# Kernel tuning notes

Measured on AMD Instinct MI355X. Metric: run time of the kernel, lower is better.

## Reference

```python
import math
import jax, jax.numpy as jnp
import numpy as np

SCORE_THR = 0.05
NMS_THR = 0.5
MIN_SIZE = 0.01
MAX_DET = 100
SCALE_CLAMP = math.log(1000.0 / 16.0)
WX, WY, WW, WH = 10.0, 10.0, 5.0, 5.0  # BoxCoder weights


def setup_inputs() -> dict:
    key = jax.random.key(0)
    k1, k2, k3, k4 = jax.random.split(key, 4)
    B, N, C = 4, 2048, 3
    H = W = 800
    class_logits = 2.0 * jax.random.normal(k1, (B, N, C), dtype=jnp.float32)
    box_regression = 0.5 * jax.random.normal(k2, (B, N, 4 * C), dtype=jnp.float32)
    cxy = jax.random.uniform(k3, (B, N, 2), minval=0.0, maxval=float(W))
    wh = jax.random.uniform(k4, (B, N, 2), minval=4.0, maxval=100.0)
    proposals = jnp.concatenate([cxy - 0.5 * wh, cxy + 0.5 * wh], axis=-1)
    proposals = jnp.clip(proposals, 0.0, float(W))
    return {"class_logits": class_logits, "box_regression": box_regression,
            "proposals": proposals, "image_h": H, "image_w": W}


def _decode(rel, props):
    # rel: [N, C, 4] deltas, props: [N, 4] xyxy -> [N, C, 4] decoded boxes
    w = props[:, 2] - props[:, 0]
    h = props[:, 3] - props[:, 1]
    cx = props[:, 0] + 0.5 * w
    cy = props[:, 1] + 0.5 * h
    dx = rel[..., 0] / WX
    dy = rel[..., 1] / WY
    dw = jnp.minimum(rel[..., 2] / WW, SCALE_CLAMP)
    dh = jnp.minimum(rel[..., 3] / WH, SCALE_CLAMP)
    pcx = dx * w[:, None] + cx[:, None]
    pcy = dy * h[:, None] + cy[:, None]
    pw = jnp.exp(dw) * w[:, None]
    ph = jnp.exp(dh) * h[:, None]
    return jnp.stack([pcx - 0.5 * pw, pcy - 0.5 * ph,
                      pcx + 0.5 * pw, pcy + 0.5 * ph], axis=-1)


def _pairwise_iou(b):
    # b: [M, 4] -> [M, M]
    area = (b[:, 2] - b[:, 0]) * (b[:, 3] - b[:, 1])
    lt = jnp.maximum(b[:, None, :2], b[None, :, :2])
    rb = jnp.minimum(b[:, None, 2:], b[None, :, 2:])
    whd = jnp.clip(rb - lt, 0.0)
    inter = whd[..., 0] * whd[..., 1]
    return inter / (area[:, None] + area[None, :] - inter + 1e-7)


def _per_image(logits, rel, props, H, W):
    N, C = logits.shape
    scores = jax.nn.softmax(logits, axis=-1)               # [N, C]
    boxes = _decode(rel.reshape(N, C, 4), props)           # [N, C, 4]
    # clip to image (x in [0,W], y in [0,H])
    boxes = jnp.stack([jnp.clip(boxes[..., 0], 0.0, W),
                       jnp.clip(boxes[..., 1], 0.0, H),
                       jnp.clip(boxes[..., 2], 0.0, W),
                       jnp.clip(boxes[..., 3], 0.0, H)], axis=-1)
    # drop background class and flatten -> M = N*(C-1)
    boxes = boxes[:, 1:, :].reshape(-1, 4)
    scores = scores[:, 1:].reshape(-1)
    labels = jnp.broadcast_to(jnp.arange(1, C), (N, C - 1)).reshape(-1)
    valid = ((scores > SCORE_THR)
             & (boxes[:, 2] - boxes[:, 0] >= MIN_SIZE)
             & (boxes[:, 3] - boxes[:, 1] >= MIN_SIZE))
    # batched_nms via per-class coordinate offset
    offset = labels.astype(boxes.dtype) * (jnp.max(boxes) + 1.0)
    ob = boxes + offset[:, None]
    sort_key = jnp.where(valid, scores, -jnp.inf)
    order = jnp.argsort(-sort_key)
    bs, ss, ls, vs, obs = boxes[order], scores[order], labels[order], valid[order], ob[order]
    iou = _pairwise_iou(obs)                               # [M, M]
    M = bs.shape[0]
    idxs = jnp.arange(M)
    def body(i, keep):
        sup = keep[i] & (iou[i] > NMS_THR) & (idxs > i)
        return keep & ~sup
    keep = jax.lax.fori_loop(0, M, body, vs)
    sel = jnp.argsort(~keep, stable=True)[:MAX_DET]        # kept first, score order preserved
    kb, ksc, kl, kk = bs[sel], ss[sel], ls[sel], keep[sel]
    kb = jnp.where(kk[:, None], kb, 0.0)
    ksc = jnp.where(kk, ksc, 0.0)
    kl = jnp.where(kk, kl, 0)
    return kb, ksc, kl, kk


def reference(class_logits, box_regression, proposals, image_h, image_w):
    H = jnp.float32(image_h)
    W = jnp.float32(image_w)
    f = jax.vmap(lambda l, r, p: _per_image(l, r, p, H, W))
    boxes, scores, labels, keep = f(class_logits, box_regression, proposals)
    return boxes, scores, labels, keep
```

## Files before the change

kernel.cpp:

```cpp
#include <hip/hip_runtime.h>
#include <stdint.h>

#define BB 4
#define NN 2048
#define CC 3
#define MM (NN * (CC - 1))
#define MAXDET 100
#define SCORE_THR 0.05f
#define NMS_THR 0.5f
#define MIN_SIZE 0.01f
#define TTARGET 512
#define SSKCAP 1024

#define SCORE_OFF (BB * MAXDET * 4)
#define LABEL_OFF (SCORE_OFF + BB * MAXDET)
#define KEEP_OFF (LABEL_OFF + BB * MAXDET)
#define STASH(b, j) (SCORE_OFF + (b) * MAXDET + 96 + (j))

__global__ __launch_bounds__(512) void decode_kernel(const float* __restrict__ logits,
                                                     const float* __restrict__ rel,
                                                     const float* __restrict__ props,
                                                     const int* __restrict__ ph,
                                                     const int* __restrict__ pw,
                                                     float4* __restrict__ cand_box,
                                                     unsigned long long* __restrict__ keys,
                                                     float* __restrict__ out) {
#pragma clang fp contract(off)
  __shared__ float red[512];
  int tid = threadIdx.x;
  int t = blockIdx.x * 512 + tid;
  int b = t >> 11;
  int n = t & 2047;
  float Hf = (float)ph[0];
  float Wf = (float)pw[0];

  const float* lg = logits + (size_t)t * CC;
  float l0 = lg[0], l1 = lg[1], l2 = lg[2];
  float mx = fmaxf(l0, fmaxf(l1, l2));
  float e0 = expf(l0 - mx), e1 = expf(l1 - mx), e2 = expf(l2 - mx);
  float ssum = (e0 + e1) + e2;

  float4 pr = ((const float4*)props)[t];
  float w = pr.z - pr.x, h = pr.w - pr.y;
  float cx = pr.x + 0.5f * w, cy = pr.y + 0.5f * h;
  const float4* rl = (const float4*)(rel + (size_t)t * 12);
  const float SCALE_CLAMP = 4.135166556742356f;

  float lmax = 0.0f;
  for (int c = 1; c < CC; ++c) {
    float4 rv = rl[c];
    float score = (c == 1 ? e1 : e2) / ssum;
    float dx = rv.x / 10.0f;
    float dy = rv.y / 10.0f;
    float dw = fminf(rv.z / 5.0f, SCALE_CLAMP);
    float dh = fminf(rv.w / 5.0f, SCALE_CLAMP);
    float pcx = dx * w + cx;
    float pcy = dy * h + cy;
    float bw = expf(dw) * w;
    float bh = expf(dh) * h;
    float x1 = pcx - 0.5f * bw, y1 = pcy - 0.5f * bh;
    float x2 = pcx + 0.5f * bw, y2 = pcy + 0.5f * bh;
    x1 = fminf(fmaxf(x1, 0.0f), Wf);
    y1 = fminf(fmaxf(y1, 0.0f), Hf);
    x2 = fminf(fmaxf(x2, 0.0f), Wf);
    y2 = fminf(fmaxf(y2, 0.0f), Hf);

    lmax = fmaxf(lmax, fmaxf(fmaxf(x1, y1), fmaxf(x2, y2)));

    bool valid = (score > SCORE_THR) && (x2 - x1 >= MIN_SIZE) && (y2 - y1 >= MIN_SIZE);
    int m = n * (CC - 1) + (c - 1);
    cand_box[(size_t)b * MM + m] = make_float4(x1, y1, x2, y2);
    unsigned long long key = 0ull;
    if (valid)
      key = (((unsigned long long)__float_as_uint(score)) << 32) |
            (unsigned long long)(0xFFFFFFFFu - (unsigned)m);
    keys[(size_t)b * MM + m] = key;
  }

  red[tid] = lmax;
  __syncthreads();
  for (int s2 = 256; s2 > 0; s2 >>= 1) {
    if (tid < s2) red[tid] = fmaxf(red[tid], red[tid + s2]);
    __syncthreads();
  }
  if (tid == 0) out[STASH(b, blockIdx.x & 3)] = red[0];
}

__device__ __forceinline__ int run_nms(const unsigned long long* skeys, int count,
                                       const float4* sbox, int G,
                                       const float4* __restrict__ cbg, float off_base,
                                       int b, float* __restrict__ out) {
#pragma clang fp contract(off)
  int lane = threadIdx.x;
  float4 kob0 = make_float4(0, 0, 0, 0), kob1 = make_float4(0, 0, 0, 0);
  float4 kraw0 = make_float4(0, 0, 0, 0), kraw1 = make_float4(0, 0, 0, 0);
  float karea0 = 0.0f, karea1 = 0.0f, ksc0 = 0.0f, ksc1 = 0.0f;
  int klb0 = 0, klb1 = 0;
  int cnt = 0;

  unsigned long long key0 = (count > 0) ? skeys[0] : 0ull;
  unsigned long long key1 = (count > 1) ? skeys[1] : 0ull;
  float4 bx0 = make_float4(0, 0, 0, 0);
  if (count > 0) bx0 = sbox[0];

  for (int i = 0; i < count; ++i) {
    unsigned long long key2 = (i + 2 < count) ? skeys[i + 2] : 0ull;
    float4 bx1 = make_float4(0, 0, 0, 0);
    if (i + 1 < count) {
      int m1 = (int)(0xFFFFFFFFu - (unsigned)key1);
      bx1 = (i + 1 < G) ? sbox[i + 1] : cbg[m1];
    }

    unsigned hik = (unsigned)(key0 >> 32);
    if (hik == 0u) break;
    int m = (int)(0xFFFFFFFFu - (unsigned)key0);
    int lbl = (m & 1) + 1;
    float off = (float)lbl * off_base;
    float ax1 = bx0.x + off, ay1 = bx0.y + off;
    float ax2 = bx0.z + off, ay2 = bx0.w + off;
    float aarea = (ax2 - ax1) * (ay2 - ay1);

    bool sup = false;
    if (lane < cnt) {
      float ltx = fmaxf(kob0.x, ax1), lty = fmaxf(kob0.y, ay1);
      float rbx = fminf(kob0.z, ax2), rby = fminf(kob0.w, ay2);
      float iw = fmaxf(rbx - ltx, 0.0f), ih = fmaxf(rby - lty, 0.0f);
      float inter = iw * ih;
      float denom = ((karea0 + aarea) - inter) + 1e-7f;
      if (inter / denom > NMS_THR) sup = true;
    }
    if (lane + 64 < cnt) {
      float ltx = fmaxf(kob1.x, ax1), lty = fmaxf(kob1.y, ay1);
      float rbx = fminf(kob1.z, ax2), rby = fminf(kob1.w, ay2);
      float iw = fmaxf(rbx - ltx, 0.0f), ih = fmaxf(rby - lty, 0.0f);
      float inter = iw * ih;
      float denom = ((karea1 + aarea) - inter) + 1e-7f;
      if (inter / denom > NMS_THR) sup = true;
    }
    if (!__any(sup)) {
      if (cnt < 64) {
        if (lane == cnt) {
          kob0 = make_float4(ax1, ay1, ax2, ay2);
          kraw0 = bx0;
          karea0 = aarea;
          ksc0 = __uint_as_float(hik);
          klb0 = lbl;
        }
      } else {
        if (lane == cnt - 64) {
          kob1 = make_float4(ax1, ay1, ax2, ay2);
          kraw1 = bx0;
          karea1 = aarea;
          ksc1 = __uint_as_float(hik);
          klb1 = lbl;
        }
      }
      cnt++;
      if (cnt >= MAXDET) break;
    }
    key0 = key1;
    key1 = key2;
    bx0 = bx1;
  }

  for (int r = 0; r < 2; ++r) {
    int s = r * 64 + lane;
    if (s < cnt) {
      float4 bx = r ? kraw1 : kraw0;
      float sc = r ? ksc1 : ksc0;
      int lb = r ? klb1 : klb0;
      float* obp = out + (size_t)b * MAXDET * 4 + (size_t)s * 4;
      obp[0] = bx.x; obp[1] = bx.y; obp[2] = bx.z; obp[3] = bx.w;
      out[SCORE_OFF + b * MAXDET + s] = sc;
      out[LABEL_OFF + b * MAXDET + s] = (float)lb;
      out[KEEP_OFF + b * MAXDET + s] = 1.0f;
    }
  }
  return cnt;
}

__global__ __launch_bounds__(512) void nms_kernel(const float4* __restrict__ cand_box,
                                                  const unsigned long long* __restrict__ keys,
                                                  float* __restrict__ out) {
#pragma clang fp contract(off)
  __shared__ __align__(16) unsigned long long sk[MM];
  __shared__ __align__(16) unsigned long long ssk[SSKCAP];
  __shared__ float4 sbox[SSKCAP];
  __shared__ unsigned hist[1024];
  __shared__ int s_scnt, s_thr, s_cnt, s_fb;

  int b = blockIdx.x;
  int tid = threadIdx.x;
  const float4* cbg = cand_box + (size_t)b * MM;

  {
    const ulonglong2* kp = (const ulonglong2*)(keys + (size_t)b * MM);
    ulonglong2* sp = (ulonglong2*)sk;
    for (int i = tid; i < MM / 2; i += 512) sp[i] = kp[i];
  }
  hist[tid] = 0u;
  hist[tid + 512] = 0u;
  if (tid == 0) { s_scnt = 0; s_thr = 0; s_fb = 0; s_cnt = 0; }
  float m01 = fmaxf(out[STASH(b, 0)], out[STASH(b, 1)]);
  float m23 = fmaxf(out[STASH(b, 2)], out[STASH(b, 3)]);
  float off_base = fmaxf(m01, m23) + 1.0f;
  __syncthreads();

  for (int i = tid; i < MM; i += 512) {
    unsigned hik = (unsigned)(sk[i] >> 32);
    if (hik != 0u) atomicAdd(&hist[(hik >> 16) & 1023], 1u);
  }
  __syncthreads();

  for (int d = 1; d < 1024; d <<= 1) {
    int i0 = tid, i1 = tid + 512;
    unsigned a0 = hist[i0] + ((i0 + d < 1024) ? hist[i0 + d] : 0u);
    unsigned a1 = hist[i1] + ((i1 + d < 1024) ? hist[i1 + d] : 0u);
    __syncthreads();
    hist[i0] = a0;
    hist[i1] = a1;
    __syncthreads();
  }
  int Vtot = (int)hist[0];
  {
    int i0 = tid, i1 = tid + 512;
    unsigned h0 = hist[i0], h0n = (i0 + 1 < 1024) ? hist[i0 + 1] : 0u;
    unsigned h1 = hist[i1], h1n = (i1 + 1 < 1024) ? hist[i1 + 1] : 0u;
    if (h0 >= TTARGET && h0n < TTARGET) s_thr = i0;
    if (h1 >= TTARGET && h1n < TTARGET) s_thr = i1;
  }
  __syncthreads();
  int thr = s_thr;

  for (int i = tid; i < MM; i += 512) {
    unsigned long long key = sk[i];
    unsigned hik = (unsigned)(key >> 32);
    if (hik != 0u && (int)((hik >> 16) & 1023) >= thr) {
      int pos = atomicAdd(&s_scnt, 1);
      if (pos < SSKCAP) ssk[pos] = key;
    }
  }
  __syncthreads();
  int T = s_scnt;

  if (T <= SSKCAP) {
    int P = 1;
    while (P < T) P <<= 1;
    for (int i = T + tid; i < P; i += 512) ssk[i] = 0ull;
    for (int size = 2; size <= P; size <<= 1) {
      for (int stride = size >> 1; stride > 0; stride >>= 1) {
        __syncthreads();
        for (int i = tid; i < (P >> 1); i += 512) {
          int lo = 2 * i - (i & (stride - 1));
          int hi = lo + stride;
          bool asc = ((lo & size) != 0);
          unsigned long long a = ssk[lo], bv = ssk[hi];
          if ((a > bv) == asc) { ssk[lo] = bv; ssk[hi] = a; }
        }
      }
    }
    __syncthreads();
    for (int j = tid; j < T; j += 512) {
      int m = (int)(0xFFFFFFFFu - (unsigned)ssk[j]);
      sbox[j] = cbg[m];
    }
    __syncthreads();
    if (tid < 64) {
      int cnt = run_nms(ssk, T, sbox, SSKCAP, cbg, off_base, b, out);
      if (tid == 0) {
        s_cnt = cnt;
        s_fb = (cnt < MAXDET && T < Vtot) ? 1 : 0;
      }
    }
  } else {
    if (tid == 0) s_fb = 1;
  }
  __syncthreads();

  if (s_fb) {
    for (int size = 2; size <= MM; size <<= 1) {
      for (int stride = size >> 1; stride > 0; stride >>= 1) {
        __syncthreads();
        for (int i = tid; i < (MM >> 1); i += 512) {
          int lo = 2 * i - (i & (stride - 1));
          int hi = lo + stride;
          bool asc = ((lo & size) != 0);
          unsigned long long a = sk[lo], bv = sk[hi];
          if ((a > bv) == asc) { sk[lo] = bv; sk[hi] = a; }
        }
      }
    }
    __syncthreads();
    int Gf = (Vtot < SSKCAP) ? Vtot : SSKCAP;
    for (int j = tid; j < Gf; j += 512) {
      int m = (int)(0xFFFFFFFFu - (unsigned)sk[j]);
      sbox[j] = cbg[m];
    }
    __syncthreads();
    if (tid < 64) {
      int cnt = run_nms(sk, Vtot, sbox, Gf, cbg, off_base, b, out);
      if (tid == 0) s_cnt = cnt;
    }
    __syncthreads();
  }

  int cnt = s_cnt;
  if (tid >= cnt && tid < MAXDET) {
    float* obp = out + (size_t)b * MAXDET * 4 + (size_t)tid * 4;
    obp[0] = 0.0f; obp[1] = 0.0f; obp[2] = 0.0f; obp[3] = 0.0f;
    out[SCORE_OFF + b * MAXDET + tid] = 0.0f;
    out[LABEL_OFF + b * MAXDET + tid] = 0.0f;
    out[KEEP_OFF + b * MAXDET + tid] = 0.0f;
  }
}

extern "C" void kernel_launch(void* const* d_in, const int* in_sizes, int n_in,
                              void* d_out, int out_size, void* d_ws, size_t ws_size,
                              hipStream_t stream) {
  const float* logits = (const float*)d_in[0];
  const float* rel = (const float*)d_in[1];
  const float* props = (const float*)d_in[2];
  const int* ph = (const int*)d_in[3];
  const int* pw = (const int*)d_in[4];
  float* out = (float*)d_out;

  char* ws = (char*)d_ws;
  float4* cand_box = (float4*)ws;
  unsigned long long* keys = (unsigned long long*)(ws + (size_t)BB * MM * 16);

  decode_kernel<<<16, 512, 0, stream>>>(logits, rel, props, ph, pw, cand_box, keys, out);
  nms_kernel<<<BB, 512, 0, stream>>>(cand_box, keys, out);
}
```

Before: 113.0 us.

## Keep keys in registers, use wave-level scan, ballot compaction, and cheaper sort barriers

```diff
diff --git a/kernel.cpp b/kernel.cpp
--- a/kernel.cpp
+++ b/kernel.cpp
@@ -16,6 +16,12 @@
 #define LABEL_OFF (SCORE_OFF + BB * MAXDET)
 #define KEEP_OFF (LABEL_OFF + BB * MAXDET)
 #define STASH(b, j) (SCORE_OFF + (b) * MAXDET + 96 + (j))
+
+__device__ __forceinline__ void wave_lds_sync() {
+  __builtin_amdgcn_wave_barrier();
+  __builtin_amdgcn_s_waitcnt(0xC07F);
+  __builtin_amdgcn_wave_barrier();
+}
 
 __global__ __launch_bounds__(512) void decode_kernel(const float* __restrict__ logits,
                                                      const float* __restrict__ rel,
@@ -84,6 +90,25 @@
     __syncthreads();
   }
   if (tid == 0) out[STASH(b, blockIdx.x & 3)] = red[0];
+}
+
+__device__ void bitonic_sort_desc(unsigned long long* a, int P, int tid) {
+  int prev_big = 1;
+  for (int size = 2; size <= P; size <<= 1) {
+    for (int stride = size >> 1; stride > 0; stride >>= 1) {
+      int big = (stride >= 128);
+      if (big | prev_big) __syncthreads(); else wave_lds_sync();
+      for (int i = tid; i < (P >> 1); i += 512) {
+        int lo = 2 * i - (i & (stride - 1));
+        int hi = lo + stride;
+        bool asc = ((lo & size) != 0);
+        unsigned long long x = a[lo], y = a[hi];
+        if ((x > y) == asc) { a[lo] = y; a[hi] = x; }
+      }
+      prev_big = big;
+    }
+  }
+  __syncthreads();
 }
 
 __device__ __forceinline__ int run_nms(const unsigned long long* skeys, int count,
@@ -187,17 +212,18 @@
   __shared__ __align__(16) unsigned long long ssk[SSKCAP];
   __shared__ float4 sbox[SSKCAP];
   __shared__ unsigned hist[1024];
-  __shared__ int s_scnt, s_thr, s_cnt, s_fb;
+  __shared__ int s_scnt, s_thr, s_vtot, s_cnt, s_fb;
 
   int b = blockIdx.x;
   int tid = threadIdx.x;
+  int lane = tid & 63;
   const float4* cbg = cand_box + (size_t)b * MM;
 
-  {
-    const ulonglong2* kp = (const ulonglong2*)(keys + (size_t)b * MM);
-    ulonglong2* sp = (ulonglong2*)sk;
-    for (int i = tid; i < MM / 2; i += 512) sp[i] = kp[i];
-  }
+  const ulonglong2* kg = (const ulonglong2*)(keys + (size_t)b * MM);
+  ulonglong2 kr[4];
+#pragma unroll
+  for (int j = 0; j < 4; ++j) kr[j] = kg[j * 512 + tid];
+
   hist[tid] = 0u;
   hist[tid + 512] = 0u;
   if (tid == 0) { s_scnt = 0; s_thr = 0; s_fb = 0; s_cnt = 0; }
@@ -206,37 +232,61 @@
   float off_base = fmaxf(m01, m23) + 1.0f;
   __syncthreads();
 
-  for (int i = tid; i < MM; i += 512) {
-    unsigned hik = (unsigned)(sk[i] >> 32);
-    if (hik != 0u) atomicAdd(&hist[(hik >> 16) & 1023], 1u);
-  }
-  __syncthreads();
-
-  for (int d = 1; d < 1024; d <<= 1) {
-    int i0 = tid, i1 = tid + 512;
-    unsigned a0 = hist[i0] + ((i0 + d < 1024) ? hist[i0 + d] : 0u);
-    unsigned a1 = hist[i1] + ((i1 + d < 1024) ? hist[i1 + d] : 0u);
-    __syncthreads();
-    hist[i0] = a0;
-    hist[i1] = a1;
-    __syncthreads();
-  }
-  int Vtot = (int)hist[0];
-  {
-    int i0 = tid, i1 = tid + 512;
-    unsigned h0 = hist[i0], h0n = (i0 + 1 < 1024) ? hist[i0 + 1] : 0u;
-    unsigned h1 = hist[i1], h1n = (i1 + 1 < 1024) ? hist[i1 + 1] : 0u;
-    if (h0 >= TTARGET && h0n < TTARGET) s_thr = i0;
-    if (h1 >= TTARGET && h1n < TTARGET) s_thr = i1;
+#pragma unroll
+  for (int j = 0; j < 4; ++j) {
+    unsigned h0 = (unsigned)(kr[j].x >> 32);
+    unsigned h1 = (unsigned)(kr[j].y >> 32);
+    if (h0) atomicAdd(&hist[(h0 >> 16) & 1023], 1u);
+    if (h1) atomicAdd(&hist[(h1 >> 16) & 1023], 1u);
+  }
+  __syncthreads();
+
+  if (tid < 64) {
+    unsigned own[16];
+#pragma unroll
+    for (int i = 0; i < 16; ++i) own[i] = hist[tid * 16 + i];
+    unsigned psum = 0;
+#pragma unroll
+    for (int i = 0; i < 16; ++i) psum += own[i];
+    unsigned s = psum;
+    for (int d = 1; d < 64; d <<= 1) {
+      unsigned o = __shfl_down(s, d);
+      if (tid + d < 64) s += o;
+    }
+    unsigned after = s - psum;
+    int best = -1;
+    unsigned run = after;
+#pragma unroll
+    for (int i = 15; i >= 0; --i) {
+      run += own[i];
+      if (best < 0 && run >= TTARGET) best = tid * 16 + i;
+    }
+    int gb = best;
+    for (int d = 1; d < 64; d <<= 1) {
+      int o = __shfl_down(gb, d);
+      if (tid + d < 64) gb = (o > gb) ? o : gb;
+    }
+    if (tid == 0) {
+      s_thr = (gb < 0) ? 0 : gb;
+      s_vtot = (int)s;
+    }
   }
   __syncthreads();
   int thr = s_thr;
-
-  for (int i = tid; i < MM; i += 512) {
-    unsigned long long key = sk[i];
+  int Vtot = s_vtot;
+
+#pragma unroll
+  for (int j = 0; j < 8; ++j) {
+    unsigned long long key = (j & 1) ? kr[j >> 1].y : kr[j >> 1].x;
     unsigned hik = (unsigned)(key >> 32);
-    if (hik != 0u && (int)((hik >> 16) & 1023) >= thr) {
-      int pos = atomicAdd(&s_scnt, 1);
+    bool pred = (hik != 0u) && ((int)((hik >> 16) & 1023) >= thr);
+    unsigned long long mask = __ballot(pred);
+    int ofs = __popcll(mask & ((1ull << lane) - 1ull));
+    int base = 0;
+    if (lane == 0 && mask) base = atomicAdd(&s_scnt, (int)__popcll(mask));
+    base = __shfl(base, 0);
+    if (pred) {
+      int pos = base + ofs;
       if (pos < SSKCAP) ssk[pos] = key;
     }
   }
@@ -247,22 +297,11 @@
     int P = 1;
     while (P < T) P <<= 1;
     for (int i = T + tid; i < P; i += 512) ssk[i] = 0ull;
-    for (int size = 2; size <= P; size <<= 1) {
-      for (int stride = size >> 1; stride > 0; stride >>= 1) {
-        __syncthreads();
-        for (int i = tid; i < (P >> 1); i += 512) {
-          int lo = 2 * i - (i & (stride - 1));
-          int hi = lo + stride;
-          bool asc = ((lo & size) != 0);
-          unsigned long long a = ssk[lo], bv = ssk[hi];
-          if ((a > bv) == asc) { ssk[lo] = bv; ssk[hi] = a; }
-        }
-      }
-    }
-    __syncthreads();
-    for (int j = tid; j < T; j += 512) {
-      int m = (int)(0xFFFFFFFFu - (unsigned)ssk[j]);
-      sbox[j] = cbg[m];
+    __syncthreads();
+    bitonic_sort_desc(ssk, P, tid);
+    for (int jj = tid; jj < T; jj += 512) {
+      int m = (int)(0xFFFFFFFFu - (unsigned)ssk[jj]);
+      sbox[jj] = cbg[m];
     }
     __syncthreads();
     if (tid < 64) {
@@ -278,23 +317,15 @@
   __syncthreads();
 
   if (s_fb) {
-    for (int size = 2; size <= MM; size <<= 1) {
-      for (int stride = size >> 1; stride > 0; stride >>= 1) {
-        __syncthreads();
-        for (int i = tid; i < (MM >> 1); i += 512) {
-          int lo = 2 * i - (i & (stride - 1));
-          int hi = lo + stride;
-          bool asc = ((lo & size) != 0);
-          unsigned long long a = sk[lo], bv = sk[hi];
-          if ((a > bv) == asc) { sk[lo] = bv; sk[hi] = a; }
-        }
-      }
-    }
-    __syncthreads();
+    ulonglong2* skp = (ulonglong2*)sk;
+#pragma unroll
+    for (int j = 0; j < 4; ++j) skp[j * 512 + tid] = kr[j];
+    __syncthreads();
+    bitonic_sort_desc(sk, MM, tid);
     int Gf = (Vtot < SSKCAP) ? Vtot : SSKCAP;
-    for (int j = tid; j < Gf; j += 512) {
-      int m = (int)(0xFFFFFFFFu - (unsigned)sk[j]);
-      sbox[j] = cbg[m];
+    for (int jj = tid; jj < Gf; jj += 512) {
+      int m = (int)(0xFFFFFFFFu - (unsigned)sk[jj]);
+      sbox[jj] = cbg[m];
     }
     __syncthreads();
     if (tid < 64) {
```

Measured after the change: 111.9 us. Within noise of the previous version (-0.9%).
